# Kernel optimization log

Measured on AMD Instinct MI355X. Metric: run time of the kernel, lower is better.

Reference implementation:

```python
import jax, jax.numpy as jnp
import numpy as np
from jax import lax

NUM_SAMPLES = 16
EPSILON = 1e-08
CHUNK = 1024  # tile size for the reverse NN search (matches torch batch_size)


def _cdist(a, b):
    # Euclidean distance matrix [Na, Nb] via gemm form, numerically floored for sqrt.
    d2 = (a * a).sum(-1)[:, None] + (b * b).sum(-1)[None, :] - 2.0 * (a @ b.T)
    return jnp.sqrt(jnp.maximum(d2, 1e-12))


def setup_inputs() -> dict:
    key = jax.random.key(0)
    k = jax.random.split(key, 6)
    N, F, M, G = 16384, 16384, 4096, 8192
    return {
        "original_vertices": jax.random.normal(k[0], (N, 3), dtype=jnp.float32),
        "original_faces": jax.random.randint(k[1], (F, 3), 0, N),
        "simplified_vertices": jax.random.normal(k[2], (M, 3), dtype=jnp.float32),
        "simplified_faces": jax.random.randint(k[3], (G, 3), 0, M),
        "face_probabilities": jax.random.uniform(k[4], (G,), dtype=jnp.float32),
        "r1": jax.random.uniform(k[5], (G, NUM_SAMPLES, 1), dtype=jnp.float32),
        "r2": jax.random.uniform(jax.random.fold_in(key, 7), (G, NUM_SAMPLES, 1), dtype=jnp.float32),
    }


def reference(original_vertices, original_faces, simplified_vertices,
              simplified_faces, face_probabilities, r1, r2):
    G = simplified_faces.shape[0]
    probs = face_probabilities[:G]  # pad/slice to num simplified faces (identity here)

    # ---- forward term: simplified barycenters -> nearest original barycenter ----
    orig_bary = original_vertices[original_faces].mean(axis=1)      # [F,3]
    simp_bary = simplified_vertices[simplified_faces].mean(axis=1)  # [G,3]
    min_d = _cdist(simp_bary, orig_bary).min(axis=1)                # [G]
    forward_term = (probs * min_d).sum() + 1e-4 * (1.0 - probs).sum()

    # ---- reverse term: sample points on simplified faces, NN to original verts ----
    sqrt_r1 = jnp.sqrt(r1)
    u = 1.0 - sqrt_r1
    v = sqrt_r1 * (1.0 - r2)
    w = sqrt_r1 * r2
    fv = simplified_vertices[simplified_faces]  # [G,3,3]
    pts = (u * fv[:, None, 0] + v * fv[:, None, 1] + w * fv[:, None, 2]).reshape(-1, 3)

    total = pts.shape[0]  # G * NUM_SAMPLES, divisible by CHUNK
    vsq = (original_vertices * original_vertices).sum(-1)  # [N]

    def chunk_min(p):  # p: [CHUNK, 3]
        d2 = (p * p).sum(-1)[:, None] + vsq[None, :] - 2.0 * (p @ original_vertices.T)
        return jnp.sqrt(jnp.maximum(d2, 1e-12)).min(axis=1)

    mins = lax.map(chunk_min, pts.reshape(total // CHUNK, CHUNK, 3)).reshape(-1)
    max_dist = mins.max() + EPSILON
    scaled = mins / max_dist * 0.1
    probs_exp = jnp.repeat(probs, NUM_SAMPLES)
    reverse_term = (probs_exp * scaled).sum()

    return forward_term + reverse_term
```

## Files before the change

### kernel.cpp

```cpp
#include <hip/hip_runtime.h>
#include <math.h>

constexpr int N_V  = 16384;
constexpr int N_F  = 16384;
constexpr int G_F  = 8192;
constexpr int NS   = 16;
constexpr int NPTS = G_F * NS;

constexpr int MB    = 2;
constexpr int TILES = 32;

typedef _Float16 half8 __attribute__((ext_vector_type(8)));
typedef float    f32x16 __attribute__((ext_vector_type(16)));

constexpr int F4_ACC   = 0;
constexpr int F4_SB    = 1;
constexpr int F4_PTS   = F4_SB + G_F;
constexpr int F4_PKV   = F4_PTS + NPTS;
constexpr int F4_PKO   = F4_PKV + 32768;
constexpr int F4_TOTAL = F4_PKO + 32768;
constexpr int WS_MINF  = F4_TOTAL * 4;
constexpr int WS_MINR  = WS_MINF + G_F;

__device__ __forceinline__ void mfma4(half8 a0, half8 a1, half8 cA, half8 cB,
                                      f32x16& d0A, f32x16& d0B,
                                      f32x16& d1A, f32x16& d1B) {
  asm("v_mfma_f32_32x32x16_f16 %0, %4, %6, 0\n\t"
      "v_mfma_f32_32x32x16_f16 %1, %4, %7, 0\n\t"
      "v_mfma_f32_32x32x16_f16 %2, %5, %6, 0\n\t"
      "v_mfma_f32_32x32x16_f16 %3, %5, %7, 0\n\t"
      "s_nop 7\n\t"
      "s_nop 7\n\t"
      "s_nop 7\n\t"
      "s_nop 7\n\t"
      "s_nop 7\n\t"
      "s_nop 7"
      : "=&v"(d0A), "=&v"(d0B), "=&v"(d1A), "=&v"(d1B)
      : "v"(a0), "v"(a1), "v"(cA), "v"(cB));
}

__device__ __forceinline__ void pack_target(float x, float y, float z, float sq,
                                            half8* __restrict__ pk, int tile, int n) {
  float ax = -2.0f*x, ay = -2.0f*y, az = -2.0f*z;
  _Float16 hx = (_Float16)ax, hy = (_Float16)ay, hz = (_Float16)az, hw = (_Float16)sq;
  _Float16 lx = (_Float16)(ax - (float)hx), ly = (_Float16)(ay - (float)hy);
  _Float16 lz = (_Float16)(az - (float)hz), lw = (_Float16)(sq - (float)hw);
  half8 h0; h0[0]=hx; h0[1]=hy; h0[2]=hz; h0[3]=hw; h0[4]=lx; h0[5]=ly; h0[6]=lz; h0[7]=lw;
  half8 h1; h1[0]=hx; h1[1]=hy; h1[2]=hz; h1[3]=hw;
  h1[4]=(_Float16)0.0f; h1[5]=(_Float16)0.0f; h1[6]=(_Float16)0.0f; h1[7]=(_Float16)0.0f;
  pk[(size_t)tile*64 + n]      = h0;
  pk[(size_t)tile*64 + 32 + n] = h1;
}

__global__ void k_prep(const float* __restrict__ ov, const int* __restrict__ of,
                       const float* __restrict__ sv, const int* __restrict__ sf,
                       const float* __restrict__ r1, const float* __restrict__ r2,
                       unsigned int* __restrict__ ws, float4* __restrict__ ws4) {
  int i = blockIdx.x * blockDim.x + threadIdx.x;
  if (i < 4) ws[i] = 0u;
  ws[WS_MINR + i] = 0x7f800000u;

  {
    int g = i >> 4;
    int a = sf[3*g], b = sf[3*g+1], c = sf[3*g+2];
    float sr = sqrtf(r1[i]);
    float u = 1.0f - sr;
    float v = sr * (1.0f - r2[i]);
    float w = sr * r2[i];
    float px = u*sv[3*a]   + v*sv[3*b]   + w*sv[3*c];
    float py = u*sv[3*a+1] + v*sv[3*b+1] + w*sv[3*c+1];
    float pz = u*sv[3*a+2] + v*sv[3*b+2] + w*sv[3*c+2];
    (ws4 + F4_PTS)[i] = make_float4(px, py, pz, fmaf(px, px, fmaf(py, py, pz*pz)));
  }
  if (i < G_F) {
    ws[WS_MINF + i] = 0x7f800000u;
    int a = sf[3*i], b = sf[3*i+1], c = sf[3*i+2];
    float x = (sv[3*a] + sv[3*b] + sv[3*c]) * (1.0f/3.0f);
    float y = (sv[3*a+1] + sv[3*b+1] + sv[3*c+1]) * (1.0f/3.0f);
    float z = (sv[3*a+2] + sv[3*b+2] + sv[3*c+2]) * (1.0f/3.0f);
    (ws4 + F4_SB)[i] = make_float4(x, y, z, fmaf(x, x, fmaf(y, y, z*z)));
  }
  if (i < N_V) {
    float x = ov[3*i], y = ov[3*i+1], z = ov[3*i+2];
    pack_target(x, y, z, fmaf(x, x, fmaf(y, y, z*z)),
                (half8*)(ws4 + F4_PKV), i >> 5, i & 31);
  }
  if (i < N_F) {
    int a = of[3*i], b = of[3*i+1], c = of[3*i+2];
    float x = (ov[3*a] + ov[3*b] + ov[3*c]) * (1.0f/3.0f);
    float y = (ov[3*a+1] + ov[3*b+1] + ov[3*c+1]) * (1.0f/3.0f);
    float z = (ov[3*a+2] + ov[3*b+2] + ov[3*c+2]) * (1.0f/3.0f);
    pack_target(x, y, z, fmaf(x, x, fmaf(y, y, z*z)),
                (half8*)(ws4 + F4_PKO), i >> 5, i & 31);
  }
}

__global__ __launch_bounds__(256, 3) void k_min(const float4* __restrict__ q4,
                                                const half8* __restrict__ pk,
                                                unsigned int* __restrict__ minU,
                                                int nchunks) {
  __shared__ half8 sB[TILES * 64];
  int lane  = threadIdx.x & 63;
  int wave  = threadIdx.x >> 6;
  int half_ = lane >> 5;
  int m     = lane & 31;
  int qbase = blockIdx.x * 256 + wave * (32 * MB);
  int tbase = blockIdx.y * nchunks * TILES;

  half8 afrag[MB];
  float psq[MB];
  #pragma unroll
  for (int mb = 0; mb < MB; ++mb) {
    float4 q = q4[qbase + mb*32 + m];
    psq[mb] = q.w;
    _Float16 hx = (_Float16)q.x, hy = (_Float16)q.y, hz = (_Float16)q.z;
    half8 a;
    if (half_ == 0) {
      a[0]=hx; a[1]=hy; a[2]=hz; a[3]=(_Float16)1.0f;
      a[4]=hx; a[5]=hy; a[6]=hz; a[7]=(_Float16)1.0f;
    } else {
      a[0]=(_Float16)(q.x-(float)hx); a[1]=(_Float16)(q.y-(float)hy);
      a[2]=(_Float16)(q.z-(float)hz); a[3]=(_Float16)0.0f;
      a[4]=(_Float16)0.0f; a[5]=(_Float16)0.0f; a[6]=(_Float16)0.0f; a[7]=(_Float16)0.0f;
    }
    afrag[mb] = a;
  }

  float inf = __uint_as_float(0x7f800000u);
  float rm[MB][16];
  #pragma unroll
  for (int mb = 0; mb < MB; ++mb)
    #pragma unroll
    for (int r = 0; r < 16; ++r) rm[mb][r] = inf;

  for (int ch = 0; ch < nchunks; ++ch) {
    int t0 = tbase + ch * TILES;
    if (ch > 0) __syncthreads();
    const half8* src = pk + (size_t)(t0 + wave) * 64 + lane;
    #pragma unroll
    for (int j = 0; j < TILES/4; ++j) {
      __builtin_amdgcn_global_load_lds(
          (const __attribute__((address_space(1))) unsigned int*)(src + (size_t)j*256),
          (__attribute__((address_space(3))) unsigned int*)&sB[(wave + 4*j) * 64],
          16, 0, 0);
    }
    __syncthreads();

    for (int t = 0; t < TILES; t += 2) {
      half8 cA = sB[t*64 + lane];
      half8 cB = sB[t*64 + 64 + lane];
      f32x16 dA, dB, eA, eB;
      mfma4(afrag[0], afrag[1], cA, cB, dA, dB, eA, eB);
      #pragma unroll
      for (int r = 0; r < 16; ++r)
        rm[0][r] = fminf(fminf(rm[0][r], dA[r]), dB[r]);
      #pragma unroll
      for (int r = 0; r < 16; ++r)
        rm[1][r] = fminf(fminf(rm[1][r], eA[r]), eB[r]);
    }
  }

  #pragma unroll
  for (int mb = 0; mb < MB; ++mb) {
    #pragma unroll
    for (int r = 0; r < 16; ++r) {
      float v = rm[mb][r];
      v = fminf(v, __shfl_xor(v, 1, 64));
      v = fminf(v, __shfl_xor(v, 2, 64));
      v = fminf(v, __shfl_xor(v, 4, 64));
      v = fminf(v, __shfl_xor(v, 8, 64));
      v = fminf(v, __shfl_xor(v, 16, 64));
      int row = (r & 3) + 8*(r >> 2) + 4*half_;
      if (m == row) {
        float d2 = fmaxf(psq[mb] + v, 0.0f);
        atomicMin(&minU[qbase + mb*32 + m], __float_as_uint(d2));
      }
    }
  }
}

__device__ __forceinline__ float waveSum(float v) {
  #pragma unroll
  for (int o = 32; o > 0; o >>= 1) v += __shfl_down(v, o, 64);
  return v;
}
__device__ __forceinline__ float waveMax(float v) {
  #pragma unroll
  for (int o = 32; o > 0; o >>= 1) v = fmaxf(v, __shfl_down(v, o, 64));
  return v;
}

__global__ void k_reduce(const float* __restrict__ probs, const float* __restrict__ minf,
                         const float* __restrict__ minr, float* __restrict__ acc) {
  int tid = blockIdx.x * blockDim.x + threadIdx.x;
  int stride = gridDim.x * blockDim.x;
  float sf = 0.0f, sr = 0.0f, mx = 0.0f;
  for (int i = tid; i < NPTS; i += stride) {
    float d = sqrtf(fmaxf(minr[i], 1e-12f));
    sr = fmaf(probs[i >> 4], d, sr);
    mx = fmaxf(mx, d);
    if (i < G_F) {
      float df = sqrtf(fmaxf(minf[i], 1e-12f));
      sf = fmaf(probs[i], df, sf);
      sf = fmaf(1e-4f, 1.0f - probs[i], sf);
    }
  }
  __shared__ float lf[4], lr[4], lm[4];
  int lane = threadIdx.x & 63, wid = threadIdx.x >> 6;
  sf = waveSum(sf); sr = waveSum(sr); mx = waveMax(mx);
  if (lane == 0) { lf[wid] = sf; lr[wid] = sr; lm[wid] = mx; }
  __syncthreads();
  if (wid == 0) {
    float a = (lane < 4) ? lf[lane] : 0.0f;
    float b = (lane < 4) ? lr[lane] : 0.0f;
    float c = (lane < 4) ? lm[lane] : 0.0f;
    a = waveSum(a); b = waveSum(b); c = waveMax(c);
    if (lane == 0) {
      atomicAdd(&acc[0], a);
      atomicAdd(&acc[1], b);
      atomicMax((unsigned int*)&acc[2], __float_as_uint(c));
    }
  }
}

__global__ void k_final(const float* __restrict__ acc, float* __restrict__ out) {
  float maxd = acc[2] + 1e-8f;
  out[0] = acc[0] + acc[1] * 0.1f / maxd;
}

extern "C" void kernel_launch(void* const* d_in, const int* in_sizes, int n_in,
                              void* d_out, int out_size, void* d_ws, size_t ws_size,
                              hipStream_t stream) {
  const float* ov    = (const float*)d_in[0];
  const int*   of    = (const int*)  d_in[1];
  const float* sv    = (const float*)d_in[2];
  const int*   sfc   = (const int*)  d_in[3];
  const float* probs = (const float*)d_in[4];
  const float* r1    = (const float*)d_in[5];
  const float* r2    = (const float*)d_in[6];
  float*  ws  = (float*)d_ws;
  float4* ws4 = (float4*)d_ws;
  float*  out = (float*)d_out;

  float*        acc   = ws;
  float4*       sb4   = ws4 + F4_SB;
  float4*       pts4  = ws4 + F4_PTS;
  half8*        pkV   = (half8*)(ws4 + F4_PKV);
  half8*        pkO   = (half8*)(ws4 + F4_PKO);
  unsigned int* minfU = (unsigned int*)(ws + WS_MINF);
  unsigned int* minrU = (unsigned int*)(ws + WS_MINR);
  const float*  minfF = ws + WS_MINF;
  const float*  minrF = ws + WS_MINR;

  k_prep<<<NPTS/256, 256, 0, stream>>>(ov, of, sv, sfc, r1, r2,
                                       (unsigned int*)ws, ws4);
  k_min<<<dim3(G_F/256, 16), 256, 0, stream>>>(sb4, pkO, minfU, 1);
  k_min<<<dim3(NPTS/256, 8), 256, 0, stream>>>(pts4, pkV, minrU, 2);
  k_reduce<<<256, 256, 0, stream>>>(probs, minfF, minrF, acc);
  k_final<<<1, 1, 0, stream>>>(acc, out);
}
```

Baseline: 183.8 us.

## Double-buffer LDS target tiles and prefetch fragments in NN-min kernel

Splits each block's target range into smaller 16-tile chunks held in a two-slot LDS buffer, issuing the async global-to-LDS load for the next chunk before computing on the current one. The first chunk's load is started before the query fragments are built. Inside the chunk, the next pair of B fragments is read from LDS ahead of the MFMA calls, and an empty asm keeps the running minima in vector registers. Launch chunk counts double to cover the same targets. The aim is to hide global-load latency behind MFMA work. The price is more barriers and one extra LDS buffer, and correctness depends on the single barrier per iteration fencing both the reuse of a buffer and the async load landing.

```diff
diff --git a/kernel.cpp b/kernel.cpp
--- a/kernel.cpp
+++ b/kernel.cpp
@@ -8,7 +8,7 @@
 constexpr int NPTS = G_F * NS;
 
 constexpr int MB    = 2;
-constexpr int TILES = 32;
+constexpr int CT    = 16;
 
 typedef _Float16 half8 __attribute__((ext_vector_type(8)));
 typedef float    f32x16 __attribute__((ext_vector_type(16)));
@@ -99,13 +99,24 @@
                                                 const half8* __restrict__ pk,
                                                 unsigned int* __restrict__ minU,
                                                 int nchunks) {
-  __shared__ half8 sB[TILES * 64];
+  __shared__ half8 sB[2][CT * 64];
   int lane  = threadIdx.x & 63;
   int wave  = threadIdx.x >> 6;
   int half_ = lane >> 5;
   int m     = lane & 31;
   int qbase = blockIdx.x * 256 + wave * (32 * MB);
-  int tbase = blockIdx.y * nchunks * TILES;
+  int tbase = blockIdx.y * nchunks * CT;
+
+  {
+    const half8* src = pk + (size_t)(tbase + wave) * 64 + lane;
+    #pragma unroll
+    for (int j = 0; j < CT/4; ++j) {
+      __builtin_amdgcn_global_load_lds(
+          (const __attribute__((address_space(1))) unsigned int*)(src + (size_t)j*256),
+          (__attribute__((address_space(3))) unsigned int*)&sB[0][(wave + 4*j) * 64],
+          16, 0, 0);
+    }
+  }
 
   half8 afrag[MB];
   float psq[MB];
@@ -127,36 +138,43 @@
   }
 
   float inf = __uint_as_float(0x7f800000u);
-  float rm[MB][16];
-  #pragma unroll
-  for (int mb = 0; mb < MB; ++mb)
+  f32x16 rm0, rm1;
+  #pragma unroll
+  for (int r = 0; r < 16; ++r) { rm0[r] = inf; rm1[r] = inf; }
+
+  for (int ch = 0; ch < nchunks; ++ch) {
+    const int b = ch & 1;
+    __syncthreads();
+    if (ch + 1 < nchunks) {
+      const half8* src = pk + (size_t)(tbase + (ch+1)*CT + wave) * 64 + lane;
+      #pragma unroll
+      for (int j = 0; j < CT/4; ++j) {
+        __builtin_amdgcn_global_load_lds(
+            (const __attribute__((address_space(1))) unsigned int*)(src + (size_t)j*256),
+            (__attribute__((address_space(3))) unsigned int*)&sB[b^1][(wave + 4*j) * 64],
+            16, 0, 0);
+      }
+    }
+
+    half8 cA = sB[b][lane];
+    half8 cB = sB[b][64 + lane];
     #pragma unroll
-    for (int r = 0; r < 16; ++r) rm[mb][r] = inf;
-
-  for (int ch = 0; ch < nchunks; ++ch) {
-    int t0 = tbase + ch * TILES;
-    if (ch > 0) __syncthreads();
-    const half8* src = pk + (size_t)(t0 + wave) * 64 + lane;
-    #pragma unroll
-    for (int j = 0; j < TILES/4; ++j) {
-      __builtin_amdgcn_global_load_lds(
-          (const __attribute__((address_space(1))) unsigned int*)(src + (size_t)j*256),
-          (__attribute__((address_space(3))) unsigned int*)&sB[(wave + 4*j) * 64],
-          16, 0, 0);
-    }
-    __syncthreads();
-
-    for (int t = 0; t < TILES; t += 2) {
-      half8 cA = sB[t*64 + lane];
-      half8 cB = sB[t*64 + 64 + lane];
+    for (int t = 0; t < CT; t += 2) {
+      half8 nA, nB;
+      if (t < CT - 2) {
+        nA = sB[b][(t+2)*64 + lane];
+        nB = sB[b][(t+3)*64 + lane];
+      }
       f32x16 dA, dB, eA, eB;
       mfma4(afrag[0], afrag[1], cA, cB, dA, dB, eA, eB);
       #pragma unroll
       for (int r = 0; r < 16; ++r)
-        rm[0][r] = fminf(fminf(rm[0][r], dA[r]), dB[r]);
+        rm0[r] = fminf(fminf(rm0[r], dA[r]), dB[r]);
       #pragma unroll
       for (int r = 0; r < 16; ++r)
-        rm[1][r] = fminf(fminf(rm[1][r], eA[r]), eB[r]);
+        rm1[r] = fminf(fminf(rm1[r], eA[r]), eB[r]);
+      asm("" : "+v"(rm0), "+v"(rm1));
+      if (t < CT - 2) { cA = nA; cB = nB; }
     }
   }
 
@@ -164,7 +182,7 @@
   for (int mb = 0; mb < MB; ++mb) {
     #pragma unroll
     for (int r = 0; r < 16; ++r) {
-      float v = rm[mb][r];
+      float v = (mb == 0) ? rm0[r] : rm1[r];
       v = fminf(v, __shfl_xor(v, 1, 64));
       v = fminf(v, __shfl_xor(v, 2, 64));
       v = fminf(v, __shfl_xor(v, 4, 64));
@@ -254,8 +272,8 @@
 
   k_prep<<<NPTS/256, 256, 0, stream>>>(ov, of, sv, sfc, r1, r2,
                                        (unsigned int*)ws, ws4);
-  k_min<<<dim3(G_F/256, 16), 256, 0, stream>>>(sb4, pkO, minfU, 1);
-  k_min<<<dim3(NPTS/256, 8), 256, 0, stream>>>(pts4, pkV, minrU, 2);
+  k_min<<<dim3(G_F/256, 16), 256, 0, stream>>>(sb4, pkO, minfU, 2);
+  k_min<<<dim3(NPTS/256, 8), 256, 0, stream>>>(pts4, pkV, minrU, 4);
   k_reduce<<<256, 256, 0, stream>>>(probs, minfF, minrF, acc);
   k_final<<<1, 1, 0, stream>>>(acc, out);
 }
```

After: 180.1 us. 1.02x faster.
